# Performance work log

Measured on AMD Instinct MI355X. Metric: run time of the kernel, lower is better.

Reference implementation:

```python
import math
import jax, jax.numpy as jnp
import numpy as np
from jax import lax

B, L, D = 8, 4096, 512
H, DK, DV = 8, 64, 64
FACTOR = 1

def setup_inputs() -> dict:
    key = jax.random.key(0)
    ks = jax.random.split(key, 7)
    Q = jax.random.normal(ks[0], (B, L, D), dtype=jnp.float32)
    K = jax.random.normal(ks[1], (B, L, D), dtype=jnp.float32)
    V = jax.random.normal(ks[2], (B, L, D), dtype=jnp.float32)
    s = 0.02
    WQ = jax.random.normal(ks[3], (D, H * DK), dtype=jnp.float32) * s
    WK = jax.random.normal(ks[4], (D, H * DK), dtype=jnp.float32) * s
    WV = jax.random.normal(ks[5], (D, H * DV), dtype=jnp.float32) * s
    Wfc = jax.random.normal(ks[6], (H * DV, D), dtype=jnp.float32) * s
    attn_mask = jnp.zeros((1,), dtype=bool)  # ignored by AutoCorrelation branch
    return {"Q": Q, "K": K, "V": V, "attn_mask": attn_mask,
            "WQ": WQ, "WK": WK, "WV": WV, "Wfc": Wfc}

def _autocorrelation(q, k, v):
    # q, k, v: [B, L, H, E] -> permute to [B, H, E, L]
    qp = q.transpose(0, 2, 3, 1)
    kp = k.transpose(0, 2, 3, 1)
    vp = v.transpose(0, 2, 3, 1)
    l = qp.shape[-1]
    qf = jnp.fft.rfft(qp, axis=-1)
    kf = jnp.fft.rfft(kp, axis=-1)
    corr = jnp.fft.irfft(qf * jnp.conj(kf), n=l, axis=-1)  # [B,H,E,L]
    top_k = int(FACTOR * math.log(l))  # static: depends on shape only
    # training-mode aggregation: global delays from batch-averaged correlation
    mean_value = corr.mean(axis=1).mean(axis=1)              # [B, L]
    index = lax.top_k(mean_value.mean(axis=0), top_k)[1]     # [top_k]
    weights = mean_value[:, index]                           # [B, top_k]
    tmp_corr = jax.nn.softmax(weights, axis=-1)              # [B, top_k]
    ar = jnp.arange(l)
    delays_agg = jnp.zeros_like(vp)
    for i in range(top_k):  # small fixed loop (top_k = 8)
        idx = (ar + index[i]) % l  # == torch.roll(v, -index[i], -1)
        delays_agg = delays_agg + vp[..., idx] * tmp_corr[:, i][:, None, None, None]
    return delays_agg.transpose(0, 3, 1, 2)  # [B, L, H, E]

def reference(Q, K, V, attn_mask, WQ, WK, WV, Wfc):
    b = Q.shape[0]
    q = (Q @ WQ).reshape(b, -1, H, DK)  # [B,L,H,dk]
    k = (K @ WK).reshape(b, -1, H, DK)
    v = (V @ WV).reshape(b, -1, H, DV)
    context = _autocorrelation(q, k, v)        # [B,L,H,dv]
    context = context.reshape(b, -1, H * DV)   # [B,L,H*dv]
    return context @ Wfc                       # [B,L,d_model]
```

## Files before the change

kernel.cpp:

```cpp
#include <hip/hip_runtime.h>
#include <math.h>
#include <utility>

#define B 8
#define L 4096
#define C 512
#define NF 4096
#define TOPK 8
#define TS 272
#define CPBK 8
#define NBLK (B * C / CPBK)

typedef short bf16x8 __attribute__((ext_vector_type(8)));
typedef float f32x4 __attribute__((ext_vector_type(4)));

__device__ inline unsigned short f2bf(float f) {
    unsigned int u = __float_as_uint(f);
    u += 0x7FFF + ((u >> 16) & 1);
    return (unsigned short)(u >> 16);
}
__device__ inline float bf2f(unsigned short h) {
    return __uint_as_float(((unsigned int)h) << 16);
}

__device__ inline void gload_lds16(const void* g, void* l) {
    __builtin_amdgcn_global_load_lds(
        (const __attribute__((address_space(1))) void*)g,
        (__attribute__((address_space(3))) void*)l, 16, 0, 0);
}

__global__ __launch_bounds__(256) void cvt_bf16_3(const float4* __restrict__ i0,
                                                  uint4* __restrict__ o0,
                                                  const float4* __restrict__ i1,
                                                  uint4* __restrict__ o1,
                                                  const float4* __restrict__ i2,
                                                  uint4* __restrict__ o2) {
    const float4* in = blockIdx.z == 0 ? i0 : (blockIdx.z == 1 ? i1 : i2);
    uint4* out       = blockIdx.z == 0 ? o0 : (blockIdx.z == 1 ? o1 : o2);
    const int gid = blockIdx.x * 256 + threadIdx.x;
    const float4 a = in[gid * 2];
    const float4 b = in[gid * 2 + 1];
    uint4 o;
    o.x = (unsigned)f2bf(a.x) | ((unsigned)f2bf(a.y) << 16);
    o.y = (unsigned)f2bf(a.z) | ((unsigned)f2bf(a.w) << 16);
    o.z = (unsigned)f2bf(b.x) | ((unsigned)f2bf(b.y) << 16);
    o.w = (unsigned)f2bf(b.z) | ((unsigned)f2bf(b.w) << 16);
    out[gid] = o;
}

__global__ __launch_bounds__(256) void ktrans(const float* __restrict__ Kin,
                                              unsigned short* __restrict__ kTb) {
    __shared__ float tile[64][65];
    const int t0 = blockIdx.x * 64;
    const int c0 = blockIdx.y * 64;
    const int b  = blockIdx.z;
    const int tid = threadIdx.x;
    const int tc = tid & 63, tr = tid >> 6;
#pragma unroll
    for (int i = 0; i < 16; ++i) {
        const int r = tr + i * 4;
        tile[r][tc] = Kin[((size_t)(b * 4096) + t0 + r) * 512 + c0 + tc];
    }
    __syncthreads();
#pragma unroll
    for (int i = 0; i < 16; ++i) {
        const int cc = tr + i * 4;
        kTb[((size_t)(b * 512) + c0 + cc) * 4096 + t0 + tc] = f2bf(tile[tc][cc]);
    }
}

__global__ __launch_bounds__(256) void wtrans(const float* __restrict__ W,
                                              unsigned short* __restrict__ Wt) {
    __shared__ float t[32][33];
    const int tx = threadIdx.x & 31, ty = threadIdx.x >> 5;
    const int bx = blockIdx.x;
    const int by = blockIdx.y;
#pragma unroll
    for (int i = 0; i < 4; ++i) {
        const int k = by * 32 + ty + i * 8;
        t[ty + i * 8][tx] = W[(size_t)k * 512 + bx * 32 + tx];
    }
    __syncthreads();
#pragma unroll
    for (int i = 0; i < 4; ++i) {
        const int n = bx * 32 + ty + i * 8;
        Wt[(size_t)n * 512 + by * 32 + tx] = f2bf(t[tx][ty + i * 8]);
    }
}

template <int TRANSOUT, int F32A>
__device__ __forceinline__ void gemm_body(unsigned short* Asm, unsigned short* Bsm,
                                          const void* __restrict__ Ap,
                                          const unsigned short* __restrict__ Bt,
                                          void* __restrict__ OutP,
                                          int row0, int col0) {
    const int tid = threadIdx.x;
    const int lane = tid & 63;
    const int w = tid >> 6;
    const int wr = w >> 1, wc = w & 1;

    const int ldr = tid >> 3;
    const int ldk = (tid & 7) << 3;
    const int ldsbase = (w << 3) * 64;

    f32x4 acc[4][4] = {};

    for (int k0 = 0; k0 < 512; k0 += 64) {
        __syncthreads();
#pragma unroll
        for (int i = 0; i < 4; ++i) {
            if (F32A) {
                const float* Af = (const float*)Ap;
                const size_t base = (size_t)(row0 + i * 32 + ldr) * 512 + k0 + ldk;
                const float4 v0 = *(const float4*)&Af[base];
                const float4 v1 = *(const float4*)&Af[base + 4];
                ushort4 u0, u1;
                u0.x = f2bf(v0.x); u0.y = f2bf(v0.y); u0.z = f2bf(v0.z); u0.w = f2bf(v0.w);
                u1.x = f2bf(v1.x); u1.y = f2bf(v1.y); u1.z = f2bf(v1.z); u1.w = f2bf(v1.w);
                *(ushort4*)&Asm[i * 2048 + ldr * 64 + ldk]     = u0;
                *(ushort4*)&Asm[i * 2048 + ldr * 64 + ldk + 4] = u1;
            } else {
                gload_lds16((const unsigned short*)Ap +
                                (size_t)(row0 + i * 32 + ldr) * 512 + k0 + ldk,
                            Asm + i * 32 * 64 + ldsbase);
            }
            gload_lds16(Bt + (size_t)(col0 + i * 32 + ldr) * 512 + k0 + ldk,
                        Bsm + i * 32 * 64 + ldsbase);
        }
        __syncthreads();
#pragma unroll
        for (int kk = 0; kk < 2; ++kk) {
            bf16x8 af[4], bfv[4];
#pragma unroll
            for (int m = 0; m < 4; ++m)
                af[m] = *(const bf16x8*)&Asm[(wr * 64 + m * 16 + (lane & 15)) * 64 +
                                             kk * 32 + (lane >> 4) * 8];
#pragma unroll
            for (int n = 0; n < 4; ++n)
                bfv[n] = *(const bf16x8*)&Bsm[(wc * 64 + n * 16 + (lane & 15)) * 64 +
                                              kk * 32 + (lane >> 4) * 8];
#pragma unroll
            for (int m = 0; m < 4; ++m)
#pragma unroll
                for (int n = 0; n < 4; ++n)
                    acc[m][n] = __builtin_amdgcn_mfma_f32_16x16x32_bf16(
                        af[m], bfv[n], acc[m][n], 0, 0, 0);
        }
    }

    if (TRANSOUT) {
        unsigned short* Out = (unsigned short*)OutP;
        const int bidx = row0 >> 12;
        const int t0base = (row0 & 4095) + wr * 64 + (lane >> 4) * 4;
#pragma unroll
        for (int n = 0; n < 4; ++n) {
            const int col = col0 + wc * 64 + n * 16 + (lane & 15);
#pragma unroll
            for (int m = 0; m < 4; ++m) {
                const int t0 = t0base + m * 16;
                ushort4 v;
                v.x = f2bf(acc[m][n][0]);
                v.y = f2bf(acc[m][n][1]);
                v.z = f2bf(acc[m][n][2]);
                v.w = f2bf(acc[m][n][3]);
                *(ushort4*)&Out[((size_t)(bidx * 512 + col)) * 4096 + t0] = v;
            }
        }
    } else {
#pragma unroll
        for (int m = 0; m < 4; ++m) {
            const int rbase = row0 + wr * 64 + m * 16 + (lane >> 4) * 4;
#pragma unroll
            for (int n = 0; n < 4; ++n) {
                const int col = col0 + wc * 64 + n * 16 + (lane & 15);
#pragma unroll
                for (int j = 0; j < 4; ++j)
                    ((unsigned short*)OutP)[(size_t)(rbase + j) * 512 + col] =
                        f2bf(acc[m][n][j]);
            }
        }
    }
}

template <int TRANSOUT, int F32A>
__global__ __launch_bounds__(256) void gemm_mfma(const void* __restrict__ Ap,
                                                 const unsigned short* __restrict__ Bt,
                                                 void* __restrict__ OutP) {
    __shared__ __align__(16) unsigned short Asm[128 * 64];
    __shared__ __align__(16) unsigned short Bsm[128 * 64];
    gemm_body<TRANSOUT, F32A>(Asm, Bsm, Ap, Bt, OutP,
                              blockIdx.x * 128, blockIdx.y * 128);
}

__global__ __launch_bounds__(256) void gemm_mini2(const unsigned short* __restrict__ A0,
                                                  const unsigned short* __restrict__ B0,
                                                  unsigned short* __restrict__ O0,
                                                  const unsigned short* __restrict__ A1,
                                                  const unsigned short* __restrict__ B1,
                                                  unsigned short* __restrict__ O1) {
    __shared__ __align__(16) unsigned short Asm[128 * 64];
    __shared__ __align__(16) unsigned short Bsm[128 * 64];
    const unsigned short* Ap = blockIdx.z ? A1 : A0;
    const unsigned short* Bt = blockIdx.z ? B1 : B0;
    unsigned short* Out      = blockIdx.z ? O1 : O0;
    gemm_body<0, 0>(Asm, Bsm, Ap, Bt, Out, blockIdx.x * 128, blockIdx.y * 128);
}

constexpr double d_sin_t(double x) {
    double t = x, s = x; const double x2 = x * x;
    for (int i = 1; i < 10; ++i) { t *= -x2 / ((2.0 * i) * (2.0 * i + 1.0)); s += t; }
    return s;
}
constexpr double d_cos_t(double x) {
    double t = 1.0, s = 1.0; const double x2 = x * x;
    for (int i = 1; i < 10; ++i) { t *= -x2 / ((2.0 * i - 1.0) * (2.0 * i)); s += t; }
    return s;
}
struct TwTab {
    float c[64]; float s[64];
    constexpr TwTab() : c{}, s{} {
        for (int j = 0; j < 64; ++j) {
            const int q = j >> 4, r = j & 15;
            const double x = 6.283185307179586476925286766559 * r / 64.0;
            const double cc = d_cos_t(x), ss = d_sin_t(x);
            double cv, sv;
            if (q == 0)      { cv =  cc; sv =  ss; }
            else if (q == 1) { cv = -ss; sv =  cc; }
            else if (q == 2) { cv = -cc; sv = -ss; }
            else             { cv =  ss; sv = -cc; }
            c[j] = (float)cv; s[j] = (float)sv;
        }
    }
};
constexpr TwTab TW;

__device__ __host__ constexpr int perm16(int p) {
    return ((p & 3) << 2) | ((p >> 2) & 3);
}

template <int E, int SGN>
__device__ __forceinline__ void twmul(float& xr, float& xi) {
    if constexpr ((E & 63) != 0) {
        constexpr float wc = TW.c[E & 63];
        constexpr float ws = (SGN < 0) ? -TW.s[E & 63] : TW.s[E & 63];
        const float r  = xr * wc - xi * ws;
        const float i2 = xr * ws + xi * wc;
        xr = r; xi = i2;
    }
}

template <int E1, int E2, int E3, int SGN>
__device__ __forceinline__ void bf4(float& ar, float& ai, float& br, float& bi,
                                    float& cr, float& ci, float& er, float& ei) {
    const float t0r = ar + cr, t0i = ai + ci, t1r = ar - cr, t1i = ai - ci;
    const float t2r = br + er, t2i = bi + ei, t3r = br - er, t3i = bi - ei;
    ar = t0r + t2r; ai = t0i + t2i;
    float x2r = t0r - t2r, x2i = t0i - t2i;
    float x1r, x1i, x3r, x3i;
    if (SGN < 0) { x1r = t1r + t3i; x1i = t1i - t3r; x3r = t1r - t3i; x3i = t1i + t3r; }
    else         { x1r = t1r - t3i; x1i = t1i + t3r; x3r = t1r + t3i; x3i = t1i - t3r; }
    twmul<E1, SGN>(x1r, x1i);
    twmul<E2, SGN>(x2r, x2i);
    twmul<E3, SGN>(x3r, x3i);
    br = x1r; bi = x1i;
    cr = x2r; ci = x2i;
    er = x3r; ei = x3i;
}

template <int SGN, int... Is>
__device__ __forceinline__ void fft16_s0(float* dr, float* di, std::integer_sequence<int, Is...>) {
    (bf4<4 * Is, 8 * Is, 12 * Is, SGN>(dr[Is], di[Is], dr[Is + 4], di[Is + 4],
                                       dr[Is + 8], di[Is + 8], dr[Is + 12], di[Is + 12]), ...);
}
template <int SGN, int... Is>
__device__ __forceinline__ void fft16_s1(float* dr, float* di, std::integer_sequence<int, Is...>) {
    (bf4<0, 0, 0, SGN>(dr[4 * Is], di[4 * Is], dr[4 * Is + 1], di[4 * Is + 1],
                       dr[4 * Is + 2], di[4 * Is + 2], dr[4 * Is + 3], di[4 * Is + 3]), ...);
}
template <int SGN>
__device__ __forceinline__ void fft16r(float* dr, float* di) {
    fft16_s0<SGN>(dr, di, std::make_integer_sequence<int, 4>{});
    fft16_s1<SGN>(dr, di, std::make_integer_sequence<int, 4>{});
}

template <int SGN>
__device__ __forceinline__ void rtw(float& xr, float& xi, float arev) {
    const float f = arev - floorf(arev);
    const float s = __builtin_amdgcn_sinf(f);
    const float c = __builtin_amdgcn_cosf(f);
    float r, i2;
    if (SGN < 0) { r = xr * c + xi * s; i2 = xi * c - xr * s; }
    else         { r = xr * c - xi * s; i2 = xi * c + xr * s; }
    xr = r; xi = i2;
}

__global__ __launch_bounds__(256) void corr_fft16(const unsigned short* __restrict__ qT,
                                                  const unsigned short* __restrict__ kT,
                                                  float* __restrict__ Ppart) {
    __shared__ float tre[16 * TS];
    __shared__ float tim[16 * TS];
    const int tid = threadIdx.x;
    const int b = blockIdx.x / (NBLK / B);
    const int local = blockIdx.x % (NBLK / B);
    const int hi = tid >> 4, lo = tid & 15;
    const int c0 = local * CPBK;

    float dr[16], di[16], aR[16], aI[16];
    unsigned short puq[16], puk[16];
#pragma unroll
    for (int p = 0; p < 16; ++p) { aR[p] = 0.f; aI[p] = 0.f; }

    {
        const unsigned short* qrow = qT + ((size_t)(b * C + c0)) * L;
        const unsigned short* krow = kT + ((size_t)(b * C + c0)) * L;
#pragma unroll
        for (int n1 = 0; n1 < 16; ++n1) {
            dr[n1] = bf2f(qrow[n1 * 256 + tid]);
            di[n1] = bf2f(krow[(4096 - n1 * 256 - tid) & 4095]);
        }
    }

#pragma unroll 1
    for (int cc = 0; cc < CPBK; ++cc) {
        if (cc + 1 < CPBK) {
            const unsigned short* qrow = qT + ((size_t)(b * C + c0 + cc + 1)) * L;
            const unsigned short* krow = kT + ((size_t)(b * C + c0 + cc + 1)) * L;
#pragma unroll
            for (int n1 = 0; n1 < 16; ++n1) {
                puq[n1] = qrow[n1 * 256 + tid];
                puk[n1] = krow[(4096 - n1 * 256 - tid) & 4095];
            }
        }
        fft16r<-1>(dr, di);
#pragma unroll
        for (int p = 1; p < 16; ++p)
            rtw<-1>(dr[p], di[p], (float)(tid * perm16(p)) * (1.0f / 4096.0f));
        __syncthreads();
#pragma unroll
        for (int p = 0; p < 16; ++p) {
            const int a = perm16(p) * TS + hi * 17 + lo;
            tre[a] = dr[p]; tim[a] = di[p];
        }
        __syncthreads();
#pragma unroll
        for (int q = 0; q < 16; ++q) {
            const int a = hi * TS + q * 17 + lo;
            dr[q] = tre[a]; di[q] = tim[a];
        }
        fft16r<-1>(dr, di);
#pragma unroll
        for (int p = 1; p < 16; ++p)
            rtw<-1>(dr[p], di[p], (float)(lo * perm16(p)) * (1.0f / 256.0f));
        __syncthreads();
#pragma unroll
        for (int p = 0; p < 16; ++p) {
            const int a = hi * TS + perm16(p) * 17 + lo;
            tre[a] = dr[p]; tim[a] = di[p];
        }
        __syncthreads();
#pragma unroll
        for (int q = 0; q < 16; ++q) {
            const int a = hi * TS + lo * 17 + q;
            dr[q] = tre[a]; di[q] = tim[a];
        }
        fft16r<-1>(dr, di);
#pragma unroll
        for (int p = 0; p < 16; ++p) {
            aR[p] += dr[p] * dr[p] - di[p] * di[p];
            aI[p] += 2.0f * dr[p] * di[p];
        }
        if (cc + 1 < CPBK) {
#pragma unroll
            for (int n1 = 0; n1 < 16; ++n1) {
                dr[n1] = bf2f(puq[n1]);
                di[n1] = bf2f(puk[n1]);
            }
        }
    }

    float* dst = Ppart + (size_t)blockIdx.x * (2 * NF);
#pragma unroll
    for (int p = 0; p < 16; ++p) {
        const int a = tid + (perm16(p) << 8);
        *(float2*)&dst[2 * a] = make_float2(aR[p], aI[p]);
    }
}

__global__ __launch_bounds__(256) void reduce_pacc(const float* __restrict__ Ppart,
                                                   float* __restrict__ Pacc) {
    const int e = blockIdx.x * 256 + threadIdx.x;
    const int b = e >> 13;
    const int j = e & 8191;
    const float* src = Ppart + (size_t)b * (NBLK / B) * (2 * NF) + j;
    float s = 0.f;
#pragma unroll 4
    for (int g = 0; g < NBLK / B; ++g) s += src[(size_t)g * (2 * NF)];
    Pacc[e] = s;
}

__global__ __launch_bounds__(256) void ifft_mean(const float* __restrict__ Pacc,
                                                 float* __restrict__ mean_value) {
    __shared__ float tre[16 * TS];
    __shared__ float tim[16 * TS];
    const int tid = threadIdx.x;
    const int b = blockIdx.x;
    const int hi = tid >> 4, lo = tid & 15;
    const float* src = Pacc + (size_t)b * (2 * NF);

    float dr[16], di[16];
#pragma unroll
    for (int n1 = 0; n1 < 16; ++n1) {
        const int a = ((tid & 15) << 4) | (tid >> 4) | (n1 << 8);
        dr[n1] = src[2 * a]; di[n1] = src[2 * a + 1];
    }
    fft16r<1>(dr, di);
#pragma unroll
    for (int p = 1; p < 16; ++p)
        rtw<1>(dr[p], di[p], (float)(tid * perm16(p)) * (1.0f / 4096.0f));
#pragma unroll
    for (int p = 0; p < 16; ++p) {
        const int a = perm16(p) * TS + hi * 17 + lo;
        tre[a] = dr[p]; tim[a] = di[p];
    }
    __syncthreads();
#pragma unroll
    for (int q = 0; q < 16; ++q) {
        const int a = hi * TS + q * 17 + lo;
        dr[q] = tre[a]; di[q] = tim[a];
    }
    fft16r<1>(dr, di);
#pragma unroll
    for (int p = 1; p < 16; ++p)
        rtw<1>(dr[p], di[p], (float)(lo * perm16(p)) * (1.0f / 256.0f));
    __syncthreads();
#pragma unroll
    for (int p = 0; p < 16; ++p) {
        const int a = hi * TS + perm16(p) * 17 + lo;
        tre[a] = dr[p]; tim[a] = di[p];
    }
    __syncthreads();
#pragma unroll
    for (int q = 0; q < 16; ++q) {
        const int a = hi * TS + lo * 17 + q;
        dr[q] = tre[a]; di[q] = tim[a];
    }
    fft16r<1>(dr, di);

    const float scale = 1.0f / (2.0f * 4096.0f * 512.0f);
#pragma unroll
    for (int p = 0; p < 16; ++p) {
        const int k = hi + (lo << 4) + (perm16(p) << 8);
        mean_value[(size_t)b * NF + k] = di[p] * scale;
    }
}

__global__ __launch_bounds__(256) void topk_softmax(const float* __restrict__ mean_value,
                                                    int* __restrict__ idx_out,
                                                    float* __restrict__ tc_out) {
    __shared__ float mv[NF];
    __shared__ float rv[256];
    __shared__ int ri[256];
    __shared__ int sel[TOPK];
    const int tid = threadIdx.x;

    for (int j = 0; j < 16; ++j) {
        const int t = j * 256 + tid;
        float s = 0.f;
        for (int b = 0; b < B; ++b) s += mean_value[(size_t)b * NF + t];
        mv[t] = s * (1.0f / (float)B);
    }
    __syncthreads();

    for (int iter = 0; iter < TOPK; ++iter) {
        float bv = -INFINITY; int bi = NF;
        for (int j = 0; j < 16; ++j) {
            const int t = j * 256 + tid;
            const float v = mv[t];
            if (v > bv || (v == bv && t < bi)) { bv = v; bi = t; }
        }
        rv[tid] = bv; ri[tid] = bi;
        __syncthreads();
        for (int off = 128; off > 0; off >>= 1) {
            if (tid < off) {
                if (rv[tid + off] > rv[tid] ||
                    (rv[tid + off] == rv[tid] && ri[tid + off] < ri[tid])) {
                    rv[tid] = rv[tid + off]; ri[tid] = ri[tid + off];
                }
            }
            __syncthreads();
        }
        if (tid == 0) { sel[iter] = ri[0]; mv[ri[0]] = -INFINITY; }
        __syncthreads();
    }

    if (tid < B) {
        float wv[TOPK];
        float mx = -INFINITY;
        for (int i = 0; i < TOPK; ++i) {
            wv[i] = mean_value[(size_t)tid * NF + sel[i]];
            mx = fmaxf(mx, wv[i]);
        }
        float sum = 0.f;
        for (int i = 0; i < TOPK; ++i) { wv[i] = expf(wv[i] - mx); sum += wv[i]; }
        const float inv = 1.0f / sum;
        for (int i = 0; i < TOPK; ++i) tc_out[tid * TOPK + i] = wv[i] * inv;
    }
    if (tid < TOPK) idx_out[tid] = sel[tid];
}

__global__ __launch_bounds__(256) void context_out(const unsigned short* __restrict__ Y,
                                                   const int* __restrict__ idx,
                                                   const float* __restrict__ tc,
                                                   float* __restrict__ out) {
    const size_t gid = (size_t)blockIdx.x * 256 + threadIdx.x;
    const int c8 = (int)(gid & 63);
    const int t  = (int)((gid >> 6) & 4095);
    const int b  = (int)(gid >> 18);

    __shared__ int sIdx[TOPK];
    __shared__ float sW[TOPK];
    if (threadIdx.x < TOPK) {
        sIdx[threadIdx.x] = idx[threadIdx.x];
        sW[threadIdx.x]   = tc[b * TOPK + threadIdx.x];
    }
    __syncthreads();

    const unsigned short* yb = Y + (size_t)b * L * C;
    float a[8] = {};
#pragma unroll
    for (int i = 0; i < TOPK; ++i) {
        const int row = (t + sIdx[i]) & (L - 1);
        const uint4 v = *(const uint4*)&yb[(size_t)row * C + c8 * 8];
        const float wgt = sW[i];
        a[0] += wgt * bf2f((unsigned short)(v.x & 0xFFFF));
        a[1] += wgt * bf2f((unsigned short)(v.x >> 16));
        a[2] += wgt * bf2f((unsigned short)(v.y & 0xFFFF));
        a[3] += wgt * bf2f((unsigned short)(v.y >> 16));
        a[4] += wgt * bf2f((unsigned short)(v.z & 0xFFFF));
        a[5] += wgt * bf2f((unsigned short)(v.z >> 16));
        a[6] += wgt * bf2f((unsigned short)(v.w & 0xFFFF));
        a[7] += wgt * bf2f((unsigned short)(v.w >> 16));
    }
    float* o = out + gid * 8;
    *(float4*)&o[0] = make_float4(a[0], a[1], a[2], a[3]);
    *(float4*)&o[4] = make_float4(a[4], a[5], a[6], a[7]);
}

extern "C" void kernel_launch(void* const* d_in, const int* in_sizes, int n_in,
                              void* d_out, int out_size, void* d_ws, size_t ws_size,
                              hipStream_t stream) {
    const float* Q   = (const float*)d_in[0];
    const float* K   = (const float*)d_in[1];
    const float* V   = (const float*)d_in[2];
    const float* WQ  = (const float*)d_in[4];
    const float* WK  = (const float*)d_in[5];
    const float* WV  = (const float*)d_in[6];
    const float* Wfc = (const float*)d_in[7];
    float* out = (float*)d_out;

    const size_t SZ = (size_t)B * L * C;
    const size_t WSZ = 512 * 512;
    unsigned short* kTb  = (unsigned short*)d_ws;
    unsigned short* qTb  = kTb + SZ;
    unsigned short* Yb   = qTb + SZ;
    unsigned short* WQb  = Yb + SZ;
    unsigned short* WKb  = WQb + WSZ;
    unsigned short* WVb  = WKb + WSZ;
    unsigned short* Wfct = WVb + WSZ;
    unsigned short* Mt   = Wfct + WSZ;
    unsigned short* Nt   = Mt + WSZ;
    float* Ppart      = (float*)(Nt + WSZ);
    float* Pacc       = Ppart + (size_t)NBLK * 2 * NF;
    float* mean_value = Pacc + (size_t)B * 2 * NF;
    float* tc         = mean_value + (size_t)B * NF;
    int*   idx        = (int*)(tc + B * TOPK);

    cvt_bf16_3<<<dim3(128, 1, 3), 256, 0, stream>>>(
        (const float4*)WQ, (uint4*)WQb,
        (const float4*)WK, (uint4*)WKb,
        (const float4*)WV, (uint4*)WVb);
    wtrans<<<dim3(16, 16), 256, 0, stream>>>(Wfc, Wfct);
    ktrans<<<dim3(64, 8, 8), 256, 0, stream>>>(K, kTb);

    gemm_mini2<<<dim3(4, 4, 2), 256, 0, stream>>>(WKb, WQb, Mt, Wfct, WVb, Nt);
    gemm_mfma<1, 1><<<dim3(256, 4), 256, 0, stream>>>(Q, Mt, qTb);
    gemm_mfma<0, 1><<<dim3(256, 4), 256, 0, stream>>>(V, Nt, Yb);

    corr_fft16<<<dim3(NBLK), 256, 0, stream>>>(qTb, kTb, Ppart);
    reduce_pacc<<<dim3(256), 256, 0, stream>>>(Ppart, Pacc);
    ifft_mean<<<dim3(B), 256, 0, stream>>>(Pacc, mean_value);
    topk_softmax<<<dim3(1), 256, 0, stream>>>(mean_value, idx, tc);

    context_out<<<dim3(8192), 256, 0, stream>>>(Yb, idx, tc, out);
}
```

Before: 251.4 us.

## Co-schedule independent kernels via block-interleaved fused launches

Merges the K transpose with the Q projection GEMM into one launch, and the correlation FFT with the V projection GEMM into another. Each launch assigns block roles by interleaving on blockIdx modulo 5 or 3, so independent compute-bound and memory-bound work share the GPU at the same time. This also removes two kernel launches. In exchange, shared memory is sized for the larger role, which may lower occupancy for the lighter role, and the heterogeneous blocks may cause load imbalance.

Result: slower. 291.2 us (+15.9%).

```diff
diff --git a/kernel.cpp b/kernel.cpp
--- a/kernel.cpp
+++ b/kernel.cpp
@@ -48,24 +48,22 @@
     out[gid] = o;
 }
 
-__global__ __launch_bounds__(256) void ktrans(const float* __restrict__ Kin,
-                                              unsigned short* __restrict__ kTb) {
-    __shared__ float tile[64][65];
-    const int t0 = blockIdx.x * 64;
-    const int c0 = blockIdx.y * 64;
-    const int b  = blockIdx.z;
+__device__ __forceinline__ void ktrans_body(float* tile,
+                                            const float* __restrict__ Kin,
+                                            unsigned short* __restrict__ kTb,
+                                            int t0, int c0, int b) {
     const int tid = threadIdx.x;
     const int tc = tid & 63, tr = tid >> 6;
 #pragma unroll
     for (int i = 0; i < 16; ++i) {
         const int r = tr + i * 4;
-        tile[r][tc] = Kin[((size_t)(b * 4096) + t0 + r) * 512 + c0 + tc];
+        tile[r * 65 + tc] = Kin[((size_t)(b * 4096) + t0 + r) * 512 + c0 + tc];
     }
     __syncthreads();
 #pragma unroll
     for (int i = 0; i < 16; ++i) {
         const int cc = tr + i * 4;
-        kTb[((size_t)(b * 512) + c0 + cc) * 4096 + t0 + tc] = f2bf(tile[tc][cc]);
+        kTb[((size_t)(b * 512) + c0 + cc) * 4096 + t0 + tc] = f2bf(tile[tc * 65 + cc]);
     }
 }
 
@@ -182,16 +180,6 @@
     }
 }
 
-template <int TRANSOUT, int F32A>
-__global__ __launch_bounds__(256) void gemm_mfma(const void* __restrict__ Ap,
-                                                 const unsigned short* __restrict__ Bt,
-                                                 void* __restrict__ OutP) {
-    __shared__ __align__(16) unsigned short Asm[128 * 64];
-    __shared__ __align__(16) unsigned short Bsm[128 * 64];
-    gemm_body<TRANSOUT, F32A>(Asm, Bsm, Ap, Bt, OutP,
-                              blockIdx.x * 128, blockIdx.y * 128);
-}
-
 __global__ __launch_bounds__(256) void gemm_mini2(const unsigned short* __restrict__ A0,
                                                   const unsigned short* __restrict__ B0,
                                                   unsigned short* __restrict__ O0,
@@ -294,14 +282,14 @@
     xr = r; xi = i2;
 }
 
-__global__ __launch_bounds__(256) void corr_fft16(const unsigned short* __restrict__ qT,
-                                                  const unsigned short* __restrict__ kT,
-                                                  float* __restrict__ Ppart) {
-    __shared__ float tre[16 * TS];
-    __shared__ float tim[16 * TS];
+__device__ __forceinline__ void corr_body(float* tre, float* tim,
+                                          const unsigned short* __restrict__ qT,
+                                          const unsigned short* __restrict__ kT,
+                                          float* __restrict__ Ppart,
+                                          int blk) {
     const int tid = threadIdx.x;
-    const int b = blockIdx.x / (NBLK / B);
-    const int local = blockIdx.x % (NBLK / B);
+    const int b = blk / (NBLK / B);
+    const int local = blk % (NBLK / B);
     const int hi = tid >> 4, lo = tid & 15;
     const int c0 = local * CPBK;
 
@@ -378,11 +366,47 @@
         }
     }
 
-    float* dst = Ppart + (size_t)blockIdx.x * (2 * NF);
+    float* dst = Ppart + (size_t)blk * (2 * NF);
 #pragma unroll
     for (int p = 0; p < 16; ++p) {
         const int a = tid + (perm16(p) << 8);
         *(float2*)&dst[2 * a] = make_float2(aR[p], aI[p]);
+    }
+}
+
+__global__ __launch_bounds__(256) void fused_a(const float* __restrict__ Q,
+                                               const unsigned short* __restrict__ Mt,
+                                               unsigned short* __restrict__ qTb,
+                                               const float* __restrict__ Kin,
+                                               unsigned short* __restrict__ kTb) {
+    __shared__ __align__(16) char smem[32768];
+    if (blockIdx.x % 5 == 0) {
+        const int id = blockIdx.x / 5;
+        unsigned short* Asm = (unsigned short*)smem;
+        unsigned short* Bsm = Asm + 128 * 64;
+        gemm_body<1, 1>(Asm, Bsm, Q, Mt, qTb, (id & 255) * 128, (id >> 8) * 128);
+    } else {
+        const int id = (blockIdx.x / 5) * 4 + (blockIdx.x % 5) - 1;
+        ktrans_body((float*)smem, Kin, kTb,
+                    (id & 63) * 64, ((id >> 6) & 7) * 64, id >> 9);
+    }
+}
+
+__global__ __launch_bounds__(256) void fused_b(const float* __restrict__ V,
+                                               const unsigned short* __restrict__ Nt,
+                                               unsigned short* __restrict__ Yb,
+                                               const unsigned short* __restrict__ qT,
+                                               const unsigned short* __restrict__ kT,
+                                               float* __restrict__ Ppart) {
+    __shared__ __align__(16) char smem[34816];
+    if (blockIdx.x % 3 == 0) {
+        const int blk = blockIdx.x / 3;
+        corr_body((float*)smem, (float*)smem + 16 * TS, qT, kT, Ppart, blk);
+    } else {
+        const int id = (blockIdx.x / 3) * 2 + (blockIdx.x % 3) - 1;
+        unsigned short* Asm = (unsigned short*)smem;
+        unsigned short* Bsm = Asm + 128 * 64;
+        gemm_body<0, 1>(Asm, Bsm, V, Nt, Yb, (id & 255) * 128, (id >> 8) * 128);
     }
 }
 
@@ -580,13 +604,12 @@
         (const float4*)WK, (uint4*)WKb,
         (const float4*)WV, (uint4*)WVb);
     wtrans<<<dim3(16, 16), 256, 0, stream>>>(Wfc, Wfct);
-    ktrans<<<dim3(64, 8, 8), 256, 0, stream>>>(K, kTb);
 
     gemm_mini2<<<dim3(4, 4, 2), 256, 0, stream>>>(WKb, WQb, Mt, Wfct, WVb, Nt);
-    gemm_mfma<1, 1><<<dim3(256, 4), 256, 0, stream>>>(Q, Mt, qTb);
-    gemm_mfma<0, 1><<<dim3(256, 4), 256, 0, stream>>>(V, Nt, Yb);
-
-    corr_fft16<<<dim3(NBLK), 256, 0, stream>>>(qTb, kTb, Ppart);
+
+    fused_a<<<dim3(5120), 256, 0, stream>>>(Q, Mt, qTb, K, kTb);
+    fused_b<<<dim3(1536), 256, 0, stream>>>(V, Nt, Yb, qTb, kTb, Ppart);
+
     reduce_pacc<<<dim3(256), 256, 0, stream>>>(Ppart, Pacc);
     ifft_mean<<<dim3(B), 256, 0, stream>>>(Pacc, mean_value);
     topk_softmax<<<dim3(1), 256, 0, stream>>>(mean_value, idx, tc);
```

## Fuse K transpose into Q projection GEMM launch via interleaved block roles

Applied to the files above, without the earlier changes.

Merges the K transpose/bf16 conversion kernel and the Q-side GEMM into one launch. Within it, every fifth block runs a GEMM tile and the other four run transpose tiles, sharing a 32KB shared buffer. The aim is to overlap the memory-bound transpose with the compute-bound GEMM and to save one launch. The trade-off is that the shared-memory footprint is sized for the larger GEMM, which may lower occupancy for the transpose blocks, and the kernels become heterogeneous.

New measurement: 261.8 us. 4.2% more time.

```diff
diff --git a/kernel.cpp b/kernel.cpp
--- a/kernel.cpp
+++ b/kernel.cpp
@@ -48,24 +48,22 @@
     out[gid] = o;
 }
 
-__global__ __launch_bounds__(256) void ktrans(const float* __restrict__ Kin,
-                                              unsigned short* __restrict__ kTb) {
-    __shared__ float tile[64][65];
-    const int t0 = blockIdx.x * 64;
-    const int c0 = blockIdx.y * 64;
-    const int b  = blockIdx.z;
+__device__ __forceinline__ void ktrans_body(float* tile,
+                                            const float* __restrict__ Kin,
+                                            unsigned short* __restrict__ kTb,
+                                            int t0, int c0, int b) {
     const int tid = threadIdx.x;
     const int tc = tid & 63, tr = tid >> 6;
 #pragma unroll
     for (int i = 0; i < 16; ++i) {
         const int r = tr + i * 4;
-        tile[r][tc] = Kin[((size_t)(b * 4096) + t0 + r) * 512 + c0 + tc];
+        tile[r * 65 + tc] = Kin[((size_t)(b * 4096) + t0 + r) * 512 + c0 + tc];
     }
     __syncthreads();
 #pragma unroll
     for (int i = 0; i < 16; ++i) {
         const int cc = tr + i * 4;
-        kTb[((size_t)(b * 512) + c0 + cc) * 4096 + t0 + tc] = f2bf(tile[tc][cc]);
+        kTb[((size_t)(b * 512) + c0 + cc) * 4096 + t0 + tc] = f2bf(tile[tc * 65 + cc]);
     }
 }
 
@@ -206,6 +204,24 @@
     gemm_body<0, 0>(Asm, Bsm, Ap, Bt, Out, blockIdx.x * 128, blockIdx.y * 128);
 }
 
+__global__ __launch_bounds__(256) void fused_a(const float* __restrict__ Q,
+                                               const unsigned short* __restrict__ Mt,
+                                               unsigned short* __restrict__ qTb,
+                                               const float* __restrict__ Kin,
+                                               unsigned short* __restrict__ kTb) {
+    __shared__ __align__(16) char smem[32768];
+    if (blockIdx.x % 5 == 0) {
+        const int id = blockIdx.x / 5;
+        unsigned short* Asm = (unsigned short*)smem;
+        unsigned short* Bsm = Asm + 128 * 64;
+        gemm_body<1, 1>(Asm, Bsm, Q, Mt, qTb, (id & 255) * 128, (id >> 8) * 128);
+    } else {
+        const int id = (blockIdx.x / 5) * 4 + (blockIdx.x % 5) - 1;
+        ktrans_body((float*)smem, Kin, kTb,
+                    (id & 63) * 64, ((id >> 6) & 7) * 64, id >> 9);
+    }
+}
+
 constexpr double d_sin_t(double x) {
     double t = x, s = x; const double x2 = x * x;
     for (int i = 1; i < 10; ++i) { t *= -x2 / ((2.0 * i) * (2.0 * i + 1.0)); s += t; }
@@ -580,10 +596,10 @@
         (const float4*)WK, (uint4*)WKb,
         (const float4*)WV, (uint4*)WVb);
     wtrans<<<dim3(16, 16), 256, 0, stream>>>(Wfc, Wfct);
-    ktrans<<<dim3(64, 8, 8), 256, 0, stream>>>(K, kTb);
 
     gemm_mini2<<<dim3(4, 4, 2), 256, 0, stream>>>(WKb, WQb, Mt, Wfct, WVb, Nt);
-    gemm_mfma<1, 1><<<dim3(256, 4), 256, 0, stream>>>(Q, Mt, qTb);
+
+    fused_a<<<dim3(5120), 256, 0, stream>>>(Q, Mt, qTb, K, kTb);
     gemm_mfma<0, 1><<<dim3(256, 4), 256, 0, stream>>>(V, Nt, Yb);
 
     corr_fft16<<<dim3(NBLK), 256, 0, stream>>>(qTb, kTb, Ppart);
```
